# Kernel optimization log

Hardware: AMD Instinct MI355X
Metric: run time of the kernel (lower is better)

Reference implementation:

```python
import jax, jax.numpy as jnp
import numpy as np

# Pangu-Weather EarthAttention3D, dim=192 branch
H = 6                 # heads
D = 192               # dim
DH = D // H           # head dim = 32
N = 2 * 6 * 12        # window tokens = 144
TW = (8 // 2) * (186 // 6)  # type_of_windows = 124
NW = 8                # number of windows (leading batch axis)
SCALE = DH ** -0.5


def setup_inputs() -> dict:
    key = jax.random.key(0)
    ks = jax.random.split(key, 7)
    return {
        "x": jax.random.normal(ks[0], (NW, TW, N, D), jnp.float32),
        "mask": jax.random.normal(ks[1], (NW, TW, N, N), jnp.float32),
        "w_qkv": jax.random.normal(ks[2], (D, 3 * D), jnp.float32) * 0.02,
        "b_qkv": jnp.zeros((3 * D,), jnp.float32),
        "bias": jax.random.normal(ks[3], (1, TW, H, N, N), jnp.float32) * 0.02,
        "w_out": jax.random.normal(ks[4], (D, D), jnp.float32) * 0.02,
        "b_out": jnp.zeros((D,), jnp.float32),
    }


def reference(x, mask, w_qkv, b_qkv, bias, w_out, b_out):
    B, W, Ntok, Dm = x.shape  # (nW, type_of_windows, win_tokens, dim)
    # fused QKV projection
    qkv = (x @ w_qkv + b_qkv).reshape(B, W, Ntok, 3, H, DH)
    qkv = jnp.transpose(qkv, (3, 0, 1, 4, 2, 5))  # (3, B, W, H, N, dh)
    q, k, v = qkv[0] * SCALE, qkv[1], qkv[2]
    # scores + earth-specific bias + window mask (broadcast over heads)
    attn = jnp.einsum('bwhnd,bwhmd->bwhnm', q, k)
    attn = attn + bias + mask[:, :, None, :, :]
    attn = jax.nn.softmax(attn, axis=-1)  # dropout_rate=0 -> identity
    out = jnp.einsum('bwhnm,bwhmd->bwhnd', attn, v)
    out = jnp.transpose(out, (0, 1, 3, 2, 4)).reshape(B, W, Ntok, Dm)
    return out @ w_out + b_out
```

## Files before the change

kernel.cpp:

```cpp
#include <hip/hip_runtime.h>
#include <hip/hip_bf16.h>

typedef __bf16 bf16_t;
typedef bf16_t bf16x8 __attribute__((ext_vector_type(8)));
typedef bf16_t bf16x4 __attribute__((ext_vector_type(4)));
typedef float f32x4 __attribute__((ext_vector_type(4)));

#define SCALE 0.17677669529663687f

#define PIN(x) asm volatile("" : "+v"(x))

__device__ __forceinline__ int swz_elem(int r, int c) {
    int g = c >> 3;
    return r * 192 + ((g >> 3) << 6) + (((g & 7) ^ (r & 7)) << 3) + (c & 7);
}

__device__ __forceinline__ void stage_chunk(bf16_t* dst, const bf16_t* src, int tid) {
#pragma unroll
    for (int it = 0; it < 3; ++it) {
        int off = (it * 256 + tid) * 8;
        __builtin_amdgcn_global_load_lds(
            (const __attribute__((address_space(1))) unsigned int*)(src + off),
            (__attribute__((address_space(3))) unsigned int*)(dst + off),
            16, 0, 0);
    }
}

__global__ void prep_weights(const float* __restrict__ w_qkv, const float* __restrict__ w_out,
                             bf16_t* __restrict__ wqkvS, bf16_t* __restrict__ woutS) {
    int i = blockIdx.x * 256 + threadIdx.x;
    if (i < 576 * 192) {
        int o = i / 192, k = i % 192;
        float v = w_qkv[k * 576 + o];
        if (o < 192) v *= SCALE;
        wqkvS[(o >> 5) * 6144 + swz_elem(o & 31, k)] = (bf16_t)v;
    }
    if (i < 192 * 192) {
        int o = i / 192, k = i % 192;
        woutS[(o >> 5) * 6144 + swz_elem(o & 31, k)] = (bf16_t)w_out[k * 192 + o];
    }
}

__global__ __launch_bounds__(256, 4)
void qkv_gemm(const float* __restrict__ x, const float* __restrict__ b_qkv,
              const bf16_t* __restrict__ wqkvS,
              bf16_t* __restrict__ Qg, bf16_t* __restrict__ Kg, bf16_t* __restrict__ Vg)
{
    __shared__ __align__(16) bf16_t Wb[2][6144];
    __shared__ __align__(16) bf16_t T[4][2][16 * 40];
    const int tid  = threadIdx.x;
    const int lane = tid & 63;
    const int wave = tid >> 6;
    const int lrow = lane & 15;
    const int lgrp = lane >> 4;
    const int r0   = blockIdx.x * 128 + wave * 32;

    stage_chunk(&Wb[0][0], wqkvS, tid);

    bf16x8 af[2][6];
#pragma unroll
    for (int tt = 0; tt < 2; ++tt)
#pragma unroll
        for (int ks = 0; ks < 6; ++ks) {
            const float* px = x + (size_t)(r0 + tt * 16 + lrow) * 192 + ks * 32 + lgrp * 8;
            f32x4 lo = *(const f32x4*)px;
            f32x4 hi = *(const f32x4*)(px + 4);
            bf16x8 v;
            v[0] = (bf16_t)lo[0]; v[1] = (bf16_t)lo[1]; v[2] = (bf16_t)lo[2]; v[3] = (bf16_t)lo[3];
            v[4] = (bf16_t)hi[0]; v[5] = (bf16_t)hi[1]; v[6] = (bf16_t)hi[2]; v[7] = (bf16_t)hi[3];
            af[tt][ks] = v;
        }
    __syncthreads();

    for (int hc = 0; hc < 18; ++hc) {
        if (hc < 17) stage_chunk(&Wb[(hc + 1) & 1][0], wqkvS + (hc + 1) * 6144, tid);
        const bf16_t* wb = &Wb[hc & 1][0];

        f32x4 a[2][2];
        a[0][0] = f32x4{0.f,0.f,0.f,0.f}; a[0][1] = f32x4{0.f,0.f,0.f,0.f};
        a[1][0] = f32x4{0.f,0.f,0.f,0.f}; a[1][1] = f32x4{0.f,0.f,0.f,0.f};
#pragma unroll
        for (int ks = 0; ks < 6; ++ks) {
            bf16x8 wf0 = *(const bf16x8*)&wb[swz_elem(lrow,      ks * 32 + lgrp * 8)];
            bf16x8 wf1 = *(const bf16x8*)&wb[swz_elem(16 + lrow, ks * 32 + lgrp * 8)];
#pragma unroll
            for (int tt = 0; tt < 2; ++tt) {
                a[tt][0] = __builtin_amdgcn_mfma_f32_16x16x32_bf16(af[tt][ks], wf0, a[tt][0], 0, 0, 0);
                a[tt][1] = __builtin_amdgcn_mfma_f32_16x16x32_bf16(af[tt][ks], wf1, a[tt][1], 0, 0, 0);
            }
        }
        __syncthreads();

        float b0 = b_qkv[hc * 32 + lrow], b1 = b_qkv[hc * 32 + 16 + lrow];
        if (hc < 6) { b0 *= SCALE; b1 *= SCALE; }
        const int h = (hc < 6) ? hc : (hc < 12) ? hc - 6 : hc - 12;
        bf16_t* dst = (hc < 6) ? Qg : (hc < 12) ? Kg : Vg;
#pragma unroll
        for (int tt = 0; tt < 2; ++tt) {
#pragma unroll
            for (int j = 0; j < 4; ++j) {
                T[wave][tt][(lgrp * 4 + j) * 40 + lrow]      = (bf16_t)(a[tt][0][j] + b0);
                T[wave][tt][(lgrp * 4 + j) * 40 + 16 + lrow] = (bf16_t)(a[tt][1][j] + b1);
            }
            bf16x8 val = *(const bf16x8*)&T[wave][tt][lrow * 40 + lgrp * 8];
            int tk = r0 + tt * 16 + lrow, bw = tk / 144, n = tk % 144;
            *(bf16x8*)&dst[((size_t)(bw * 6 + h) * 144 + n) * 32 + lgrp * 8] = val;
        }
    }
}

__global__ __launch_bounds__(256, 4)
void vt_transpose(const bf16_t* __restrict__ Vg, bf16_t* __restrict__ Vt)
{
    __shared__ bf16_t tile[4][32 * 168];
    const int lane = threadIdx.x & 63;
    const int wave = threadIdx.x >> 6;
    const int gid  = blockIdx.x * 4 + wave;
    bf16_t* tl = &tile[wave][0];
    const bf16_t* src = Vg + (size_t)gid * 4608;
    bf16_t* dst = Vt + (size_t)gid * 5120;

#pragma unroll
    for (int it = 0; it < 9; ++it) {
        int u = it * 64 + lane;
        int row = u >> 2, dc = u & 3;
        bf16x8 v = *(const bf16x8*)(src + row * 32 + dc * 8);
#pragma unroll
        for (int i = 0; i < 8; ++i) tl[(dc * 8 + i) * 168 + row] = v[i];
    }
    {
        int d = lane >> 1, c = lane & 1;
        bf16x8 z = {};
        *(bf16x8*)&tl[d * 168 + 144 + c * 8] = z;
    }
#pragma unroll
    for (int it = 0; it < 10; ++it) {
        int u = it * 64 + lane;
        int d = u / 20, c = u % 20;
        *(bf16x8*)(dst + d * 160 + c * 8) = *(const bf16x8*)&tl[d * 168 + c * 8];
    }
}

__global__ __launch_bounds__(256, 2)
void earth_attn_v6(const bf16_t* __restrict__ Qg, const bf16_t* __restrict__ Kg,
                   const bf16_t* __restrict__ Vt,
                   const float* __restrict__ mask, const float* __restrict__ bias,
                   bf16_t* __restrict__ Og)
{
    __shared__ bf16_t P[4][16 * 168];
    const int tid  = threadIdx.x;
    const int lane = tid & 63;
    const int wave = tid >> 6;
    const int lrow = lane & 15;
    const int lgrp = lane >> 4;

    const int orig = blockIdx.x;
    const int blk  = (orig & 7) * 186 + (orig >> 3);

    const int wid = blk * 4 + wave;
    const int ww  = wid / 48;
    const int r1  = wid % 48;
    const int b   = r1 / 6;
    const int h   = r1 % 6;
    const int bw  = b * 124 + ww;

    const size_t kbase = ((size_t)(bw * 6 + h) * 144) * 32;
    const size_t vbase = ((size_t)(bw * 6 + h) * 32) * 160;

    bf16x8 ka[9];
#pragma unroll
    for (int nt = 0; nt < 9; ++nt)
        ka[nt] = *(const bf16x8*)&Kg[kbase + (size_t)(nt * 16 + lrow) * 32 + lgrp * 8];

    bf16x8 va0[5], va1[5];
#pragma unroll
    for (int ks = 0; ks < 5; ++ks) {
        va0[ks] = *(const bf16x8*)&Vt[vbase + (size_t)lrow * 160 + ks * 32 + lgrp * 8];
        va1[ks] = *(const bf16x8*)&Vt[vbase + (size_t)(16 + lrow) * 160 + ks * 32 + lgrp * 8];
    }

    const float* bp_base = bias + (size_t)(ww * 6 + h) * 144 * 144;
    const float* mp_base = mask + (size_t)bw * 144 * 144;
    bf16_t* pb = &P[wave][0];
    bf16_t* ogp = Og + ((size_t)bw * 144) * 192 + h * 32 + lgrp * 8;

    bf16x8 qa = *(const bf16x8*)&Qg[kbase + (size_t)lrow * 32 + lgrp * 8];

#pragma unroll 1
    for (int t = 0; t < 9; ++t) {
        const int tn = (t < 8) ? t + 1 : 8;
        bf16x8 qa_n = *(const bf16x8*)&Qg[kbase + (size_t)(tn * 16 + lrow) * 32 + lgrp * 8];

        const float* bp = bp_base + (size_t)(t * 16 + lrow) * 144;
        const float* mp = mp_base + (size_t)(t * 16 + lrow) * 144;
        f32x4 s[9];
#pragma unroll
        for (int g = 0; g < 3; ++g) {
            f32x4 bv[3], mv[3];
#pragma unroll
            for (int i = 0; i < 3; ++i) {
                int nt = g * 3 + i;
                bv[i] = *(const f32x4*)(bp + nt * 16 + lgrp * 4);
                mv[i] = *(const f32x4*)(mp + nt * 16 + lgrp * 4);
            }
#pragma unroll
            for (int i = 0; i < 3; ++i) { PIN(bv[i]); PIN(mv[i]); }
#pragma unroll
            for (int i = 0; i < 3; ++i) {
                int nt = g * 3 + i;
                s[nt] = bv[i] + mv[i];
                s[nt] = __builtin_amdgcn_mfma_f32_16x16x32_bf16(ka[nt], qa, s[nt], 0, 0, 0);
            }
        }

        float mx = -1e30f;
#pragma unroll
        for (int nt = 0; nt < 9; ++nt)
#pragma unroll
            for (int j = 0; j < 4; ++j) mx = fmaxf(mx, s[nt][j]);
        mx = fmaxf(mx, __shfl_xor(mx, 16, 64));
        mx = fmaxf(mx, __shfl_xor(mx, 32, 64));
        float sum = 0.f;
#pragma unroll
        for (int nt = 0; nt < 9; ++nt)
#pragma unroll
            for (int j = 0; j < 4; ++j) { float e = __expf(s[nt][j] - mx); s[nt][j] = e; sum += e; }
        sum += __shfl_xor(sum, 16, 64);
        sum += __shfl_xor(sum, 32, 64);
        const float rinv = 1.0f / sum;

#pragma unroll
        for (int nt = 0; nt < 9; ++nt) {
            bf16x4 pw;
#pragma unroll
            for (int j = 0; j < 4; ++j) pw[j] = (bf16_t)(s[nt][j] * rinv);
            *(bf16x4*)&pb[lrow * 168 + nt * 16 + lgrp * 4] = pw;
        }
        {
            uint2 z2 = make_uint2(0u, 0u);
            *(uint2*)&pb[lrow * 168 + 144 + lgrp * 4] = z2;
        }

        bf16x8 pa[5];
#pragma unroll
        for (int ks = 0; ks < 5; ++ks)
            pa[ks] = *(const bf16x8*)&pb[lrow * 168 + ks * 32 + lgrp * 8];
#pragma unroll
        for (int ks = 0; ks < 5; ++ks) PIN(pa[ks]);

        f32x4 o0{0.f, 0.f, 0.f, 0.f}, o1{0.f, 0.f, 0.f, 0.f};
#pragma unroll
        for (int ks = 0; ks < 5; ++ks) {
            o0 = __builtin_amdgcn_mfma_f32_16x16x32_bf16(pa[ks], va0[ks], o0, 0, 0, 0);
            o1 = __builtin_amdgcn_mfma_f32_16x16x32_bf16(pa[ks], va1[ks], o1, 0, 0, 0);
        }

#pragma unroll
        for (int j = 0; j < 4; ++j) {
            pb[(lgrp * 4 + j) * 168 + lrow]      = (bf16_t)o0[j];
            pb[(lgrp * 4 + j) * 168 + 16 + lrow] = (bf16_t)o1[j];
        }
        bf16x8 ov = *(const bf16x8*)&pb[lrow * 168 + lgrp * 8];
        *(bf16x8*)(ogp + (size_t)(t * 16 + lrow) * 192) = ov;

        qa = qa_n;
    }
}

__global__ __launch_bounds__(256, 4)
void out_proj(const bf16_t* __restrict__ Og, const bf16_t* __restrict__ woutS,
              const float* __restrict__ b_out, float* __restrict__ out)
{
    __shared__ __align__(16) bf16_t Wb[2][6144];
    const int tid  = threadIdx.x;
    const int lane = tid & 63;
    const int wave = tid >> 6;
    const int lrow = lane & 15;
    const int lgrp = lane >> 4;
    const size_t row0 = (size_t)blockIdx.x * 64 + wave * 16;

    stage_chunk(&Wb[0][0], woutS, tid);

    bf16x8 af[6];
#pragma unroll
    for (int ks = 0; ks < 6; ++ks)
        af[ks] = *(const bf16x8*)(Og + (row0 + lrow) * 192 + ks * 32 + lgrp * 8);
    __syncthreads();

#pragma unroll
    for (int c = 0; c < 6; ++c) {
        if (c < 5) stage_chunk(&Wb[(c + 1) & 1][0], woutS + (c + 1) * 6144, tid);
        const bf16_t* wb = &Wb[c & 1][0];
        float b0 = b_out[c * 32 + lrow], b1 = b_out[c * 32 + 16 + lrow];
        f32x4 a0{b0, b0, b0, b0}, a1{b1, b1, b1, b1};
#pragma unroll
        for (int ks = 0; ks < 6; ++ks) {
            bf16x8 wf0 = *(const bf16x8*)&wb[swz_elem(lrow,      ks * 32 + lgrp * 8)];
            bf16x8 wf1 = *(const bf16x8*)&wb[swz_elem(16 + lrow, ks * 32 + lgrp * 8)];
            a0 = __builtin_amdgcn_mfma_f32_16x16x32_bf16(af[ks], wf0, a0, 0, 0, 0);
            a1 = __builtin_amdgcn_mfma_f32_16x16x32_bf16(af[ks], wf1, a1, 0, 0, 0);
        }
        __syncthreads();
#pragma unroll
        for (int j = 0; j < 4; ++j) {
            out[(row0 + lgrp * 4 + j) * 192 + c * 32 + lrow]      = a0[j];
            out[(row0 + lgrp * 4 + j) * 192 + c * 32 + 16 + lrow] = a1[j];
        }
    }
}

extern "C" void kernel_launch(void* const* d_in, const int* in_sizes, int n_in,
                              void* d_out, int out_size, void* d_ws, size_t ws_size,
                              hipStream_t stream) {
    const float* x     = (const float*)d_in[0];
    const float* mask  = (const float*)d_in[1];
    const float* w_qkv = (const float*)d_in[2];
    const float* b_qkv = (const float*)d_in[3];
    const float* bias  = (const float*)d_in[4];
    const float* w_out = (const float*)d_in[5];
    const float* b_out = (const float*)d_in[6];

    bf16_t* wqkvS = (bf16_t*)d_ws;
    bf16_t* woutS = wqkvS + 576 * 192;
    bf16_t* Qg    = woutS + 192 * 192;
    bf16_t* Kg    = Qg + (size_t)992 * 6 * 144 * 32;
    bf16_t* Vt    = Kg + (size_t)992 * 6 * 144 * 32;
    bf16_t* Og    = Vt + (size_t)992 * 6 * 32 * 160;
    bf16_t* Vg    = Og;

    prep_weights<<<dim3(432), dim3(256), 0, stream>>>(w_qkv, w_out, wqkvS, woutS);
    qkv_gemm<<<dim3(1116), dim3(256), 0, stream>>>(x, b_qkv, wqkvS, Qg, Kg, Vg);
    vt_transpose<<<dim3(1488), dim3(256), 0, stream>>>(Vg, Vt);
    earth_attn_v6<<<dim3(1488), dim3(256), 0, stream>>>(Qg, Kg, Vt, mask, bias, Og);
    out_proj<<<dim3(2232), dim3(256), 0, stream>>>(Og, woutS, b_out, (float*)d_out);
}
```

Measured before the change: 269.9 us.

## Fuse V transpose into QKV GEMM epilogue and prefetch bias/mask a tile ahead

The QKV GEMM now writes V directly in transposed, padded layout through a per-wave LDS tile, so the separate vt_transpose kernel and its extra global round trip of V are removed. The attention kernel also loads the next row-tile's bias and mask into registers while the current tile computes, instead of loading them just before the score MFMAs. The prefetch raises register pressure. The fused path no longer zeroes the Vt padding columns 144..159, so it relies on the workspace contents there being harmless.

```diff
diff --git a/kernel.cpp b/kernel.cpp
--- a/kernel.cpp
+++ b/kernel.cpp
@@ -44,10 +44,10 @@
 __global__ __launch_bounds__(256, 4)
 void qkv_gemm(const float* __restrict__ x, const float* __restrict__ b_qkv,
               const bf16_t* __restrict__ wqkvS,
-              bf16_t* __restrict__ Qg, bf16_t* __restrict__ Kg, bf16_t* __restrict__ Vg)
+              bf16_t* __restrict__ Qg, bf16_t* __restrict__ Kg, bf16_t* __restrict__ Vt)
 {
     __shared__ __align__(16) bf16_t Wb[2][6144];
-    __shared__ __align__(16) bf16_t T[4][2][16 * 40];
+    __shared__ __align__(16) bf16_t T[4][1280];
     const int tid  = threadIdx.x;
     const int lane = tid & 63;
     const int wave = tid >> 6;
@@ -72,6 +72,8 @@
         }
     __syncthreads();
 
+    bf16_t* tl = &T[wave][0];
+
     for (int hc = 0; hc < 18; ++hc) {
         if (hc < 17) stage_chunk(&Wb[(hc + 1) & 1][0], wqkvS + (hc + 1) * 6144, tid);
         const bf16_t* wb = &Wb[hc & 1][0];
@@ -93,56 +95,44 @@
 
         float b0 = b_qkv[hc * 32 + lrow], b1 = b_qkv[hc * 32 + 16 + lrow];
         if (hc < 6) { b0 *= SCALE; b1 *= SCALE; }
-        const int h = (hc < 6) ? hc : (hc < 12) ? hc - 6 : hc - 12;
-        bf16_t* dst = (hc < 6) ? Qg : (hc < 12) ? Kg : Vg;
-#pragma unroll
-        for (int tt = 0; tt < 2; ++tt) {
-#pragma unroll
-            for (int j = 0; j < 4; ++j) {
-                T[wave][tt][(lgrp * 4 + j) * 40 + lrow]      = (bf16_t)(a[tt][0][j] + b0);
-                T[wave][tt][(lgrp * 4 + j) * 40 + 16 + lrow] = (bf16_t)(a[tt][1][j] + b1);
+
+        if (hc < 12) {
+            const int h = (hc < 6) ? hc : hc - 6;
+            bf16_t* dst = (hc < 6) ? Qg : Kg;
+#pragma unroll
+            for (int tt = 0; tt < 2; ++tt) {
+#pragma unroll
+                for (int j = 0; j < 4; ++j) {
+                    tl[tt * 640 + (lgrp * 4 + j) * 40 + lrow]      = (bf16_t)(a[tt][0][j] + b0);
+                    tl[tt * 640 + (lgrp * 4 + j) * 40 + 16 + lrow] = (bf16_t)(a[tt][1][j] + b1);
+                }
+                bf16x8 val = *(const bf16x8*)&tl[tt * 640 + lrow * 40 + lgrp * 8];
+                int tk = r0 + tt * 16 + lrow, bw = tk / 144, n = tk % 144;
+                *(bf16x8*)&dst[((size_t)(bw * 6 + h) * 144 + n) * 32 + lgrp * 8] = val;
             }
-            bf16x8 val = *(const bf16x8*)&T[wave][tt][lrow * 40 + lgrp * 8];
-            int tk = r0 + tt * 16 + lrow, bw = tk / 144, n = tk % 144;
-            *(bf16x8*)&dst[((size_t)(bw * 6 + h) * 144 + n) * 32 + lgrp * 8] = val;
-        }
-    }
-}
-
-__global__ __launch_bounds__(256, 4)
-void vt_transpose(const bf16_t* __restrict__ Vg, bf16_t* __restrict__ Vt)
-{
-    __shared__ bf16_t tile[4][32 * 168];
-    const int lane = threadIdx.x & 63;
-    const int wave = threadIdx.x >> 6;
-    const int gid  = blockIdx.x * 4 + wave;
-    bf16_t* tl = &tile[wave][0];
-    const bf16_t* src = Vg + (size_t)gid * 4608;
-    bf16_t* dst = Vt + (size_t)gid * 5120;
-
-#pragma unroll
-    for (int it = 0; it < 9; ++it) {
-        int u = it * 64 + lane;
-        int row = u >> 2, dc = u & 3;
-        bf16x8 v = *(const bf16x8*)(src + row * 32 + dc * 8);
-#pragma unroll
-        for (int i = 0; i < 8; ++i) tl[(dc * 8 + i) * 168 + row] = v[i];
-    }
-    {
-        int d = lane >> 1, c = lane & 1;
-        bf16x8 z = {};
-        *(bf16x8*)&tl[d * 168 + 144 + c * 8] = z;
-    }
-#pragma unroll
-    for (int it = 0; it < 10; ++it) {
-        int u = it * 64 + lane;
-        int d = u / 20, c = u % 20;
-        *(bf16x8*)(dst + d * 160 + c * 8) = *(const bf16x8*)&tl[d * 168 + c * 8];
+        } else {
+            const int hv = hc - 12;
+#pragma unroll
+            for (int tt = 0; tt < 2; ++tt)
+#pragma unroll
+                for (int j = 0; j < 4; ++j) {
+                    tl[(lrow) * 40      + tt * 16 + lgrp * 4 + j] = (bf16_t)(a[tt][0][j] + b0);
+                    tl[(16 + lrow) * 40 + tt * 16 + lgrp * 4 + j] = (bf16_t)(a[tt][1][j] + b1);
+                }
+#pragma unroll
+            for (int it = 0; it < 2; ++it) {
+                int slot = it * 64 + lane;
+                int d = slot >> 2, c = slot & 3;
+                int tk = r0 + c * 8, bw = tk / 144, n = tk % 144;
+                bf16x8 val = *(const bf16x8*)&tl[d * 40 + c * 8];
+                *(bf16x8*)&Vt[((size_t)(bw * 6 + hv) * 32 + d) * 160 + n] = val;
+            }
+        }
     }
 }
 
 __global__ __launch_bounds__(256, 2)
-void earth_attn_v6(const bf16_t* __restrict__ Qg, const bf16_t* __restrict__ Kg,
+void earth_attn_v7(const bf16_t* __restrict__ Qg, const bf16_t* __restrict__ Kg,
                    const bf16_t* __restrict__ Vt,
                    const float* __restrict__ mask, const float* __restrict__ bias,
                    bf16_t* __restrict__ Og)
@@ -185,33 +175,41 @@
     bf16_t* ogp = Og + ((size_t)bw * 144) * 192 + h * 32 + lgrp * 8;
 
     bf16x8 qa = *(const bf16x8*)&Qg[kbase + (size_t)lrow * 32 + lgrp * 8];
+    f32x4 bv[9], mv[9];
+    {
+        const float* bp = bp_base + (size_t)lrow * 144;
+        const float* mp = mp_base + (size_t)lrow * 144;
+#pragma unroll
+        for (int nt = 0; nt < 9; ++nt) {
+            bv[nt] = *(const f32x4*)(bp + nt * 16 + lgrp * 4);
+            mv[nt] = *(const f32x4*)(mp + nt * 16 + lgrp * 4);
+        }
+    }
 
 #pragma unroll 1
     for (int t = 0; t < 9; ++t) {
+        f32x4 s[9];
+#pragma unroll
+        for (int nt = 0; nt < 9; ++nt) s[nt] = bv[nt] + mv[nt];
+
         const int tn = (t < 8) ? t + 1 : 8;
         bf16x8 qa_n = *(const bf16x8*)&Qg[kbase + (size_t)(tn * 16 + lrow) * 32 + lgrp * 8];
-
-        const float* bp = bp_base + (size_t)(t * 16 + lrow) * 144;
-        const float* mp = mp_base + (size_t)(t * 16 + lrow) * 144;
-        f32x4 s[9];
-#pragma unroll
-        for (int g = 0; g < 3; ++g) {
-            f32x4 bv[3], mv[3];
-#pragma unroll
-            for (int i = 0; i < 3; ++i) {
-                int nt = g * 3 + i;
-                bv[i] = *(const f32x4*)(bp + nt * 16 + lgrp * 4);
-                mv[i] = *(const f32x4*)(mp + nt * 16 + lgrp * 4);
+        PIN(qa_n);
+        {
+            const float* bp = bp_base + (size_t)(tn * 16 + lrow) * 144;
+            const float* mp = mp_base + (size_t)(tn * 16 + lrow) * 144;
+#pragma unroll
+            for (int nt = 0; nt < 9; ++nt) {
+                bv[nt] = *(const f32x4*)(bp + nt * 16 + lgrp * 4);
+                mv[nt] = *(const f32x4*)(mp + nt * 16 + lgrp * 4);
             }
 #pragma unroll
-            for (int i = 0; i < 3; ++i) { PIN(bv[i]); PIN(mv[i]); }
-#pragma unroll
-            for (int i = 0; i < 3; ++i) {
-                int nt = g * 3 + i;
-                s[nt] = bv[i] + mv[i];
-                s[nt] = __builtin_amdgcn_mfma_f32_16x16x32_bf16(ka[nt], qa, s[nt], 0, 0, 0);
-            }
-        }
+            for (int nt = 0; nt < 9; ++nt) { PIN(bv[nt]); PIN(mv[nt]); }
+        }
+
+#pragma unroll
+        for (int nt = 0; nt < 9; ++nt)
+            s[nt] = __builtin_amdgcn_mfma_f32_16x16x32_bf16(ka[nt], qa, s[nt], 0, 0, 0);
 
         float mx = -1e30f;
 #pragma unroll
@@ -326,11 +324,9 @@
     bf16_t* Kg    = Qg + (size_t)992 * 6 * 144 * 32;
     bf16_t* Vt    = Kg + (size_t)992 * 6 * 144 * 32;
     bf16_t* Og    = Vt + (size_t)992 * 6 * 32 * 160;
-    bf16_t* Vg    = Og;
 
     prep_weights<<<dim3(432), dim3(256), 0, stream>>>(w_qkv, w_out, wqkvS, woutS);
-    qkv_gemm<<<dim3(1116), dim3(256), 0, stream>>>(x, b_qkv, wqkvS, Qg, Kg, Vg);
-    vt_transpose<<<dim3(1488), dim3(256), 0, stream>>>(Vg, Vt);
-    earth_attn_v6<<<dim3(1488), dim3(256), 0, stream>>>(Qg, Kg, Vt, mask, bias, Og);
+    qkv_gemm<<<dim3(1116), dim3(256), 0, stream>>>(x, b_qkv, wqkvS, Qg, Kg, Vt);
+    earth_attn_v7<<<dim3(1488), dim3(256), 0, stream>>>(Qg, Kg, Vt, mask, bias, Og);
     out_proj<<<dim3(2232), dim3(256), 0, stream>>>(Og, woutS, b_out, (float*)d_out);
 }
```

Result: faster. 263.6 us (-2.3%).
